# Kernel optimization log

Measured on AMD Instinct MI355X. Metric: run time of the kernel, lower is better.

The kernel has to match this reference:

```python
import jax, jax.numpy as jnp
import numpy as np

DEPTH = 8          # complete binary tree: 2^8-1 = 255 internal nodes, 256 leaves
N_FEAT = 32
N_CLASSES = 10
BATCH = 131072


def setup_inputs() -> dict:
    key = jax.random.key(0)
    k_x, k_t, k_f, k_c = jax.random.split(key, 4)
    n_internal = (1 << DEPTH) - 1
    n_leaves = 1 << DEPTH
    x = jax.random.normal(k_x, (BATCH, N_FEAT), dtype=jnp.float32)
    # learnable per-node thresholds (initialized from the sklearn tree's thresholds)
    thresholds = jax.random.normal(k_t, (n_internal,), dtype=jnp.float32) * 0.5
    # non-differentiable split feature index per internal node
    feats = jax.random.randint(k_f, (n_internal,), 0, N_FEAT, dtype=jnp.int32)
    # majority class per leaf (argmax of sklearn value array)
    leaf_class = jax.random.randint(k_c, (n_leaves,), 0, N_CLASSES, dtype=jnp.int32)
    return {"x": x, "thresholds": thresholds, "feats": feats, "leaf_class": leaf_class}


def reference(x, thresholds, feats, leaf_class):
    # Soft decision-tree traversal. Internal nodes stored in level (heap) order:
    # level d occupies indices [2^d - 1, 2^(d+1) - 1). Children of the j-th node
    # of a level are the (2j)-th and (2j+1)-th nodes of the next level, so an
    # interleaved stack+reshape reproduces the heap child ordering exactly.
    B = x.shape[0]
    probs = jnp.ones((B, 1), dtype=x.dtype)  # root path probability
    start = 0
    for d in range(DEPTH):
        n = 1 << d
        f = feats[start:start + n]               # [n] split feature per node
        t = thresholds[start:start + n]          # [n] learnable threshold
        act = jax.nn.sigmoid(x[:, f] - t[None, :])   # [B, n] right-branch gate
        # left child gets (1 - act), right child gets act (matches _split_approx)
        probs = jnp.stack([probs * (1.0 - act), probs * act], axis=-1).reshape(B, 2 * n)
        start += n
    # sum leaf path probabilities per majority class (stack + sum in original)
    onehot = jax.nn.one_hot(leaf_class, N_CLASSES, dtype=x.dtype)  # [n_leaves, C]
    p = probs @ onehot                                             # [B, C]
    return p
```

## Files before the change

kernel.cpp:

```cpp
#include <hip/hip_runtime.h>


#define NFEAT 32
#define NCLS  10
#define TPB   256
#define RPB   128
#define XPITCH 129
#define L2E   1.4426950408889634f

typedef _Float16 f16x8 __attribute__((ext_vector_type(8)));
typedef float    f32x4 __attribute__((ext_vector_type(4)));

__device__ __forceinline__ float fexp2(float z) {
#if __has_builtin(__builtin_amdgcn_exp2f)
  return __builtin_amdgcn_exp2f(z);
#else
  return exp2f(z);
#endif
}
__device__ __forceinline__ float frcp(float z) {
#if __has_builtin(__builtin_amdgcn_rcpf)
  return __builtin_amdgcn_rcpf(z);
#else
  return 1.0f / z;
#endif
}
__device__ __forceinline__ float rlf(float v, int lane) {
  return __int_as_float(__builtin_amdgcn_readlane(__float_as_int(v), lane));
}
__device__ __forceinline__ int rli(int v, int lane) {
  return __builtin_amdgcn_readlane(v, lane);
}

struct NodeRegs {
  float ta, tb, t7;
  int   fa, fb, f7;
};

__device__ __forceinline__ void sig(float th, int ft, const float* xT, int row,
                                    float p, float& pl, float& pr) {
  const float x2 = xT[ft * XPITCH + row];
  const float e  = fexp2(th - x2);
  const float a  = frcp(1.0f + e);
  pr = p * a;
  pl = pr * e;
}
__device__ __forceinline__ void evalA(const NodeRegs& R, const float* xT, int n,
                                      int row, float p, float& pl, float& pr) {
  sig(rlf(R.ta, n), rli(R.fa, n), xT, row, p, pl, pr);
}
__device__ __forceinline__ void evalB(const NodeRegs& R, const float* xT, int n,
                                      int row, float p, float& pl, float& pr) {
  sig(rlf(R.tb, n - 63), rli(R.fb, n - 63), xT, row, p, pl, pr);
}
__device__ __forceinline__ unsigned leafpair7(const NodeRegs& R, const float* xT,
                                              int l7, int row, float p) {
  float pl, pr;
  sig(rlf(R.t7, l7), rli(R.f7, l7), xT, row, p, pl, pr);
  const _Float16 hl = (_Float16)pl, hr = (_Float16)pr;
  return ((unsigned)__builtin_bit_cast(unsigned short, hr) << 16) |
          (unsigned)__builtin_bit_cast(unsigned short, hl);
}

__device__ __forceinline__ void d5block(const NodeRegs& R, const float* xT,
                                        int row, int n5, int l7b, float p,
                                        char* rowp, int boff) {
  float pl, pr;
  evalA(R, xT, n5, row, p, pl, pr);
  float qll, qlr, qrl, qrr;
  evalB(R, xT, 2 * n5 + 1, row, pl, qll, qlr);
  evalB(R, xT, 2 * n5 + 2, row, pr, qrl, qrr);
  uint4 u;
  u.x = leafpair7(R, xT, l7b + 0, row, qll);
  u.y = leafpair7(R, xT, l7b + 1, row, qlr);
  u.z = leafpair7(R, xT, l7b + 2, row, qrl);
  u.w = leafpair7(R, xT, l7b + 3, row, qrr);
  *(uint4*)(rowp + boff) = u;
}

__global__ __launch_bounds__(TPB, 4)
void dt_kernel(const float* __restrict__ x,
               const float* __restrict__ thr,
               const int*   __restrict__ feats,
               const int*   __restrict__ leafc,
               float*       __restrict__ out) {
  __shared__ float s_xT[NFEAT * XPITCH];
  __shared__ __align__(16) char s_P[RPB * 128];
  __shared__ int s_lc[256];

  const int t    = threadIdx.x;
  const int lane = t & 63;
  const int row  = t & (RPB - 1);
  const int h    = t >> 7;

  NodeRegs R;
  R.ta = thr[lane] * L2E;
  R.tb = thr[63 + lane] * L2E;
  R.t7 = thr[127 + 64 * h + lane] * L2E;
  R.fa = feats[lane];
  R.fb = feats[63 + lane];
  R.f7 = feats[127 + 64 * h + lane];

  const float4* xg = (const float4*)x + (size_t)blockIdx.x * (RPB * NFEAT / 4);
#pragma unroll
  for (int k = 0; k < 4; ++k) {
    const int i4 = k * TPB + t;
    const float4 v = xg[i4];
    const int r  = i4 >> 3;
    const int c0 = (i4 & 7) * 4;
    s_xT[(c0 + 0) * XPITCH + r] = v.x * L2E;
    s_xT[(c0 + 1) * XPITCH + r] = v.y * L2E;
    s_xT[(c0 + 2) * XPITCH + r] = v.z * L2E;
    s_xT[(c0 + 3) * XPITCH + r] = v.w * L2E;
  }
  s_lc[t] = leafc[t];

  __syncthreads();

  float pl, pr;
  evalA(R, s_xT, 0, row, 1.0f, pl, pr);
  const float pd1 = h ? pr : pl;
  evalA(R, s_xT, 1 + h, row, pd1, pl, pr);
  const float pA = pl, pB = pr;
  float pm0, pm1, pm2, pm3;
  evalA(R, s_xT, 3 + 2 * h, row, pA, pm0, pm1);
  evalA(R, s_xT, 4 + 2 * h, row, pB, pm2, pm3);

  const int swz   = ((row ^ (row >> 3)) & 7) << 4;
  char* rowp      = s_P + row * 128;
  const int hofs  = h * 64;
  const int wv    = t >> 6;
  const int col16 = lane & 15;
  const int kgrpB = (lane >> 4) * 16;

  f32x4 acc0 = {0.f, 0.f, 0.f, 0.f};
  f32x4 acc1 = {0.f, 0.f, 0.f, 0.f};

#pragma unroll 1
  for (int p = 0; p < 4; ++p) {
    const float p3 = (p == 0) ? pm0 : (p == 1) ? pm1 : (p == 2) ? pm2 : pm3;
    const int n3 = 7 + 4 * h + p;
    float p4l, p4r;
    evalA(R, s_xT, n3, row, p3, p4l, p4r);
    float q0, q1, q2, q3;
    evalA(R, s_xT, 2 * n3 + 1, row, p4l, q0, q1);
    evalA(R, s_xT, 2 * n3 + 2, row, p4r, q2, q3);
    const int n5b = 4 * n3 + 3;
#pragma unroll
    for (int s = 0; s < 4; ++s) {
      const float q = (s == 0) ? q0 : (s == 1) ? q1 : (s == 2) ? q2 : q3;
      d5block(R, s_xT, row, n5b + s, 16 * p + 4 * s, q, rowp,
              (hofs + s * 16) ^ swz);
    }

    __syncthreads();

    f16x8 Bf0, Bf1;
    {
      const int kb = (lane >> 4) * 8;
      const int4 cA0 = *(const int4*)&s_lc[p * 32 + kb];
      const int4 cB0 = *(const int4*)&s_lc[p * 32 + kb + 4];
      uint4 u0;
      u0.x = ((cA0.x == col16) ? 0x3C00u : 0u) | (((cA0.y == col16) ? 0x3C00u : 0u) << 16);
      u0.y = ((cA0.z == col16) ? 0x3C00u : 0u) | (((cA0.w == col16) ? 0x3C00u : 0u) << 16);
      u0.z = ((cB0.x == col16) ? 0x3C00u : 0u) | (((cB0.y == col16) ? 0x3C00u : 0u) << 16);
      u0.w = ((cB0.z == col16) ? 0x3C00u : 0u) | (((cB0.w == col16) ? 0x3C00u : 0u) << 16);
      Bf0 = __builtin_bit_cast(f16x8, u0);
      const int4 cA1 = *(const int4*)&s_lc[128 + p * 32 + kb];
      const int4 cB1 = *(const int4*)&s_lc[128 + p * 32 + kb + 4];
      uint4 u1;
      u1.x = ((cA1.x == col16) ? 0x3C00u : 0u) | (((cA1.y == col16) ? 0x3C00u : 0u) << 16);
      u1.y = ((cA1.z == col16) ? 0x3C00u : 0u) | (((cA1.w == col16) ? 0x3C00u : 0u) << 16);
      u1.z = ((cB1.x == col16) ? 0x3C00u : 0u) | (((cB1.y == col16) ? 0x3C00u : 0u) << 16);
      u1.w = ((cB1.z == col16) ? 0x3C00u : 0u) | (((cB1.w == col16) ? 0x3C00u : 0u) << 16);
      Bf1 = __builtin_bit_cast(f16x8, u1);
    }

#pragma unroll
    for (int i = 0; i < 2; ++i) {
      const int arow = (wv * 2 + i) * 16 + col16;
      const int aswz = ((arow ^ (arow >> 3)) & 7) << 4;
      const char* ap = s_P + arow * 128;
      const f16x8 a0 = *(const f16x8*)(ap + ((kgrpB)      ^ aswz));
      const f16x8 a1 = *(const f16x8*)(ap + ((kgrpB + 64) ^ aswz));
      if (i == 0) {
        acc0 = __builtin_amdgcn_mfma_f32_16x16x32_f16(a0, Bf0, acc0, 0, 0, 0);
        acc0 = __builtin_amdgcn_mfma_f32_16x16x32_f16(a1, Bf1, acc0, 0, 0, 0);
      } else {
        acc1 = __builtin_amdgcn_mfma_f32_16x16x32_f16(a0, Bf0, acc1, 0, 0, 0);
        acc1 = __builtin_amdgcn_mfma_f32_16x16x32_f16(a1, Bf1, acc1, 0, 0, 0);
      }
    }

    __syncthreads();
  }

  if (col16 < NCLS) {
    const int r4 = (lane >> 4) * 4;
#pragma unroll
    for (int i = 0; i < 2; ++i) {
      const size_t gr = (size_t)blockIdx.x * RPB + (wv * 2 + i) * 16 + r4;
#pragma unroll
      for (int j = 0; j < 4; ++j) {
        out[(gr + j) * NCLS + col16] = (i == 0) ? acc0[j] : acc1[j];
      }
    }
  }
}

extern "C" void kernel_launch(void* const* d_in, const int* in_sizes, int n_in,
                              void* d_out, int out_size, void* d_ws, size_t ws_size,
                              hipStream_t stream) {
  const float* x     = (const float*)d_in[0];
  const float* thr   = (const float*)d_in[1];
  const int*   feats = (const int*)d_in[2];
  const int*   leafc = (const int*)d_in[3];
  float*       out   = (float*)d_out;

  const int B    = in_sizes[0] / NFEAT;
  const int grid = B / RPB;

  dt_kernel<<<grid, TPB, 0, stream>>>(x, thr, feats, leafc, out);
}
```

Measured before the change: 85.61 us.

## Process two rows per thread and precompute exponentials of inputs and thresholds

Each thread now handles two rows (256 rows per block) and reads both with one float2 LDS load. The sigmoid is rewritten so the exponentials of x and of the thresholds are computed once at load time, leaving one FMA and one reciprocal per node and using left = p - right. The barrier at the end of the loop moves to its start, and each wave runs four MFMA tiles instead of two. The cost is more registers, a larger LDS footprint and lower occupancy (launch bounds drop to 2). Precomputed exponentials may also overflow or underflow for extreme inputs.

```diff
diff --git a/kernel.cpp b/kernel.cpp
--- a/kernel.cpp
+++ b/kernel.cpp
@@ -4,8 +4,8 @@
 #define NFEAT 32
 #define NCLS  10
 #define TPB   256
-#define RPB   128
-#define XPITCH 129
+#define RPB   256
+#define XPITCH 258
 #define L2E   1.4426950408889634f
 
 typedef _Float16 f16x8 __attribute__((ext_vector_type(8)));
@@ -37,120 +37,140 @@
   int   fa, fb, f7;
 };
 
-__device__ __forceinline__ void sig(float th, int ft, const float* xT, int row,
-                                    float p, float& pl, float& pr) {
-  const float x2 = xT[ft * XPITCH + row];
-  const float e  = fexp2(th - x2);
-  const float a  = frcp(1.0f + e);
-  pr = p * a;
-  pl = pr * e;
-}
-__device__ __forceinline__ void evalA(const NodeRegs& R, const float* xT, int n,
-                                      int row, float p, float& pl, float& pr) {
-  sig(rlf(R.ta, n), rli(R.fa, n), xT, row, p, pl, pr);
-}
-__device__ __forceinline__ void evalB(const NodeRegs& R, const float* xT, int n,
-                                      int row, float p, float& pl, float& pr) {
-  sig(rlf(R.tb, n - 63), rli(R.fb, n - 63), xT, row, p, pl, pr);
-}
-__device__ __forceinline__ unsigned leafpair7(const NodeRegs& R, const float* xT,
-                                              int l7, int row, float p) {
-  float pl, pr;
-  sig(rlf(R.t7, l7), rli(R.f7, l7), xT, row, p, pl, pr);
-  const _Float16 hl = (_Float16)pl, hr = (_Float16)pr;
-  return ((unsigned)__builtin_bit_cast(unsigned short, hr) << 16) |
-          (unsigned)__builtin_bit_cast(unsigned short, hl);
-}
-
-__device__ __forceinline__ void d5block(const NodeRegs& R, const float* xT,
-                                        int row, int n5, int l7b, float p,
-                                        char* rowp, int boff) {
-  float pl, pr;
-  evalA(R, xT, n5, row, p, pl, pr);
-  float qll, qlr, qrl, qrr;
-  evalB(R, xT, 2 * n5 + 1, row, pl, qll, qlr);
-  evalB(R, xT, 2 * n5 + 2, row, pr, qrl, qrr);
-  uint4 u;
-  u.x = leafpair7(R, xT, l7b + 0, row, qll);
-  u.y = leafpair7(R, xT, l7b + 1, row, qlr);
-  u.z = leafpair7(R, xT, l7b + 2, row, qrl);
-  u.w = leafpair7(R, xT, l7b + 3, row, qrr);
-  *(uint4*)(rowp + boff) = u;
-}
-
-__global__ __launch_bounds__(TPB, 4)
+__device__ __forceinline__ void sig2(float tpow, int ft, const float* xT, int rp,
+                                     float p0, float p1,
+                                     float& l0, float& r0, float& l1, float& r1) {
+  const float2 w = *(const float2*)&xT[ft * XPITCH + 2 * rp];
+  const float a0 = frcp(__builtin_fmaf(tpow, w.x, 1.0f));
+  const float a1 = frcp(__builtin_fmaf(tpow, w.y, 1.0f));
+  r0 = p0 * a0;  l0 = p0 - r0;
+  r1 = p1 * a1;  l1 = p1 - r1;
+}
+__device__ __forceinline__ void evalA2(const NodeRegs& R, const float* xT, int n,
+                                       int rp, float p0, float p1,
+                                       float& l0, float& r0, float& l1, float& r1) {
+  sig2(rlf(R.ta, n), rli(R.fa, n), xT, rp, p0, p1, l0, r0, l1, r1);
+}
+__device__ __forceinline__ void evalB2(const NodeRegs& R, const float* xT, int n,
+                                       int rp, float p0, float p1,
+                                       float& l0, float& r0, float& l1, float& r1) {
+  sig2(rlf(R.tb, n - 63), rli(R.fb, n - 63), xT, rp, p0, p1, l0, r0, l1, r1);
+}
+__device__ __forceinline__ void leafpair7x2(const NodeRegs& R, const float* xT,
+                                            int l7, int rp, float p0, float p1,
+                                            unsigned& u0, unsigned& u1) {
+  float l0, r0, l1, r1;
+  sig2(rlf(R.t7, l7), rli(R.f7, l7), xT, rp, p0, p1, l0, r0, l1, r1);
+  const _Float16 hl0 = (_Float16)l0, hr0 = (_Float16)r0;
+  const _Float16 hl1 = (_Float16)l1, hr1 = (_Float16)r1;
+  u0 = ((unsigned)__builtin_bit_cast(unsigned short, hr0) << 16) |
+        (unsigned)__builtin_bit_cast(unsigned short, hl0);
+  u1 = ((unsigned)__builtin_bit_cast(unsigned short, hr1) << 16) |
+        (unsigned)__builtin_bit_cast(unsigned short, hl1);
+}
+
+__device__ __forceinline__ void d5block2(const NodeRegs& R, const float* xT,
+                                         int rp, int n5, int l7b,
+                                         float p0, float p1,
+                                         char* rowp0, char* rowp1,
+                                         int boff0, int boff1) {
+  float pl0, pr0, pl1, pr1;
+  evalA2(R, xT, n5, rp, p0, p1, pl0, pr0, pl1, pr1);
+  float qll0, qlr0, qll1, qlr1;
+  evalB2(R, xT, 2 * n5 + 1, rp, pl0, pl1, qll0, qlr0, qll1, qlr1);
+  float qrl0, qrr0, qrl1, qrr1;
+  evalB2(R, xT, 2 * n5 + 2, rp, pr0, pr1, qrl0, qrr0, qrl1, qrr1);
+  uint4 u0, u1;
+  leafpair7x2(R, xT, l7b + 0, rp, qll0, qll1, u0.x, u1.x);
+  leafpair7x2(R, xT, l7b + 1, rp, qlr0, qlr1, u0.y, u1.y);
+  leafpair7x2(R, xT, l7b + 2, rp, qrl0, qrl1, u0.z, u1.z);
+  leafpair7x2(R, xT, l7b + 3, rp, qrr0, qrr1, u0.w, u1.w);
+  *(uint4*)(rowp0 + boff0) = u0;
+  *(uint4*)(rowp1 + boff1) = u1;
+}
+
+__global__ __launch_bounds__(TPB, 2)
 void dt_kernel(const float* __restrict__ x,
                const float* __restrict__ thr,
                const int*   __restrict__ feats,
                const int*   __restrict__ leafc,
                float*       __restrict__ out) {
-  __shared__ float s_xT[NFEAT * XPITCH];
-  __shared__ __align__(16) char s_P[RPB * 128];
+  __shared__ __align__(16) float s_xT[NFEAT * XPITCH];
+  __shared__ __align__(16) char  s_P[RPB * 128];
   __shared__ int s_lc[256];
 
   const int t    = threadIdx.x;
   const int lane = t & 63;
-  const int row  = t & (RPB - 1);
+  const int rp   = t & 127;
   const int h    = t >> 7;
 
   NodeRegs R;
-  R.ta = thr[lane] * L2E;
-  R.tb = thr[63 + lane] * L2E;
-  R.t7 = thr[127 + 64 * h + lane] * L2E;
+  R.ta = fexp2(thr[lane] * L2E);
+  R.tb = fexp2(thr[63 + lane] * L2E);
+  R.t7 = fexp2(thr[127 + 64 * h + lane] * L2E);
   R.fa = feats[lane];
   R.fb = feats[63 + lane];
   R.f7 = feats[127 + 64 * h + lane];
 
   const float4* xg = (const float4*)x + (size_t)blockIdx.x * (RPB * NFEAT / 4);
 #pragma unroll
-  for (int k = 0; k < 4; ++k) {
+  for (int k = 0; k < 8; ++k) {
     const int i4 = k * TPB + t;
     const float4 v = xg[i4];
     const int r  = i4 >> 3;
     const int c0 = (i4 & 7) * 4;
-    s_xT[(c0 + 0) * XPITCH + r] = v.x * L2E;
-    s_xT[(c0 + 1) * XPITCH + r] = v.y * L2E;
-    s_xT[(c0 + 2) * XPITCH + r] = v.z * L2E;
-    s_xT[(c0 + 3) * XPITCH + r] = v.w * L2E;
+    s_xT[(c0 + 0) * XPITCH + r] = fexp2(-v.x * L2E);
+    s_xT[(c0 + 1) * XPITCH + r] = fexp2(-v.y * L2E);
+    s_xT[(c0 + 2) * XPITCH + r] = fexp2(-v.z * L2E);
+    s_xT[(c0 + 3) * XPITCH + r] = fexp2(-v.w * L2E);
   }
   s_lc[t] = leafc[t];
 
   __syncthreads();
 
-  float pl, pr;
-  evalA(R, s_xT, 0, row, 1.0f, pl, pr);
-  const float pd1 = h ? pr : pl;
-  evalA(R, s_xT, 1 + h, row, pd1, pl, pr);
-  const float pA = pl, pB = pr;
-  float pm0, pm1, pm2, pm3;
-  evalA(R, s_xT, 3 + 2 * h, row, pA, pm0, pm1);
-  evalA(R, s_xT, 4 + 2 * h, row, pB, pm2, pm3);
-
-  const int swz   = ((row ^ (row >> 3)) & 7) << 4;
-  char* rowp      = s_P + row * 128;
-  const int hofs  = h * 64;
-  const int wv    = t >> 6;
+  float pl0, pr0, pl1, pr1;
+  evalA2(R, s_xT, 0, rp, 1.0f, 1.0f, pl0, pr0, pl1, pr1);
+  const float pd10 = h ? pr0 : pl0;
+  const float pd11 = h ? pr1 : pl1;
+  evalA2(R, s_xT, 1 + h, rp, pd10, pd11, pl0, pr0, pl1, pr1);
+  const float pA0 = pl0, pB0 = pr0, pA1 = pl1, pB1 = pr1;
+  float pm00, pm01, pm02, pm03, pm10, pm11, pm12, pm13;
+  evalA2(R, s_xT, 3 + 2 * h, rp, pA0, pA1, pm00, pm01, pm10, pm11);
+  evalA2(R, s_xT, 4 + 2 * h, rp, pB0, pB1, pm02, pm03, pm12, pm13);
+
+  const int row0 = 2 * rp, row1 = row0 + 1;
+  const int swz0 = ((row0 ^ (row0 >> 3)) & 7) << 4;
+  const int swz1 = ((row1 ^ (row1 >> 3)) & 7) << 4;
+  char* rowp0    = s_P + row0 * 128;
+  char* rowp1    = s_P + row1 * 128;
+  const int hofs = h * 64;
+  const int wv   = t >> 6;
   const int col16 = lane & 15;
   const int kgrpB = (lane >> 4) * 16;
 
-  f32x4 acc0 = {0.f, 0.f, 0.f, 0.f};
-  f32x4 acc1 = {0.f, 0.f, 0.f, 0.f};
+  f32x4 acc[4];
+#pragma unroll
+  for (int i = 0; i < 4; ++i) acc[i] = (f32x4){0.f, 0.f, 0.f, 0.f};
 
 #pragma unroll 1
   for (int p = 0; p < 4; ++p) {
-    const float p3 = (p == 0) ? pm0 : (p == 1) ? pm1 : (p == 2) ? pm2 : pm3;
+    __syncthreads();
+
+    const float p30 = (p == 0) ? pm00 : (p == 1) ? pm01 : (p == 2) ? pm02 : pm03;
+    const float p31 = (p == 0) ? pm10 : (p == 1) ? pm11 : (p == 2) ? pm12 : pm13;
     const int n3 = 7 + 4 * h + p;
-    float p4l, p4r;
-    evalA(R, s_xT, n3, row, p3, p4l, p4r);
-    float q0, q1, q2, q3;
-    evalA(R, s_xT, 2 * n3 + 1, row, p4l, q0, q1);
-    evalA(R, s_xT, 2 * n3 + 2, row, p4r, q2, q3);
+    float p4l0, p4r0, p4l1, p4r1;
+    evalA2(R, s_xT, n3, rp, p30, p31, p4l0, p4r0, p4l1, p4r1);
+    float q00, q10, q01, q11, q20, q30, q21, q31;
+    evalA2(R, s_xT, 2 * n3 + 1, rp, p4l0, p4l1, q00, q10, q01, q11);
+    evalA2(R, s_xT, 2 * n3 + 2, rp, p4r0, p4r1, q20, q30, q21, q31);
     const int n5b = 4 * n3 + 3;
 #pragma unroll
     for (int s = 0; s < 4; ++s) {
-      const float q = (s == 0) ? q0 : (s == 1) ? q1 : (s == 2) ? q2 : q3;
-      d5block(R, s_xT, row, n5b + s, 16 * p + 4 * s, q, rowp,
-              (hofs + s * 16) ^ swz);
+      const float a = (s == 0) ? q00 : (s == 1) ? q10 : (s == 2) ? q20 : q30;
+      const float b = (s == 0) ? q01 : (s == 1) ? q11 : (s == 2) ? q21 : q31;
+      d5block2(R, s_xT, rp, n5b + s, 16 * p + 4 * s, a, b, rowp0, rowp1,
+               (hofs + s * 16) ^ swz0, (hofs + s * 16) ^ swz1);
     }
 
     __syncthreads();
@@ -177,32 +197,25 @@
     }
 
 #pragma unroll
-    for (int i = 0; i < 2; ++i) {
-      const int arow = (wv * 2 + i) * 16 + col16;
+    for (int i = 0; i < 4; ++i) {
+      const int arow = (wv * 4 + i) * 16 + col16;
       const int aswz = ((arow ^ (arow >> 3)) & 7) << 4;
       const char* ap = s_P + arow * 128;
       const f16x8 a0 = *(const f16x8*)(ap + ((kgrpB)      ^ aswz));
       const f16x8 a1 = *(const f16x8*)(ap + ((kgrpB + 64) ^ aswz));
-      if (i == 0) {
-        acc0 = __builtin_amdgcn_mfma_f32_16x16x32_f16(a0, Bf0, acc0, 0, 0, 0);
-        acc0 = __builtin_amdgcn_mfma_f32_16x16x32_f16(a1, Bf1, acc0, 0, 0, 0);
-      } else {
-        acc1 = __builtin_amdgcn_mfma_f32_16x16x32_f16(a0, Bf0, acc1, 0, 0, 0);
-        acc1 = __builtin_amdgcn_mfma_f32_16x16x32_f16(a1, Bf1, acc1, 0, 0, 0);
-      }
-    }
-
-    __syncthreads();
+      acc[i] = __builtin_amdgcn_mfma_f32_16x16x32_f16(a0, Bf0, acc[i], 0, 0, 0);
+      acc[i] = __builtin_amdgcn_mfma_f32_16x16x32_f16(a1, Bf1, acc[i], 0, 0, 0);
+    }
   }
 
   if (col16 < NCLS) {
     const int r4 = (lane >> 4) * 4;
 #pragma unroll
-    for (int i = 0; i < 2; ++i) {
-      const size_t gr = (size_t)blockIdx.x * RPB + (wv * 2 + i) * 16 + r4;
+    for (int i = 0; i < 4; ++i) {
+      const size_t gr = (size_t)blockIdx.x * RPB + wv * 64 + i * 16 + r4;
 #pragma unroll
       for (int j = 0; j < 4; ++j) {
-        out[(gr + j) * NCLS + col16] = (i == 0) ? acc0[j] : acc1[j];
+        out[(gr + j) * NCLS + col16] = acc[i][j];
       }
     }
   }
```

After: 82.54 us. 3.6% less time.
